# Kernel optimization log

Measured on AMD Instinct MI355X. Metric: run time of the kernel, lower is better.

Reference implementation:

```python
import jax, jax.numpy as jnp
import numpy as np

B, S, D, H = 2, 2048, 1024, 16
DK = D // H

def setup_inputs() -> dict:
    key = jax.random.key(0)
    ks = jax.random.split(key, 12)
    s = 1.0 / np.sqrt(D)
    return {
        "q": jax.random.normal(ks[0], (B, S, D), jnp.float32),
        "k": jax.random.normal(ks[1], (B, S, D), jnp.float32),
        "v": jax.random.normal(ks[2], (B, S, D), jnp.float32),
        "mask": jnp.ones((1, 1, S, S), jnp.int32),
        "Wq": jax.random.normal(ks[3], (D, D), jnp.float32) * s,
        "bq": jnp.zeros((D,), jnp.float32),
        "Wk": jax.random.normal(ks[4], (D, D), jnp.float32) * s,
        "bk": jnp.zeros((D,), jnp.float32),
        "Wv": jax.random.normal(ks[5], (D, D), jnp.float32) * s,
        "bv": jnp.zeros((D,), jnp.float32),
        "Wo": jax.random.normal(ks[6], (D, D), jnp.float32) * s,
        "bo": jnp.zeros((D,), jnp.float32),
    }

def reference(q, k, v, mask, Wq, bq, Wk, bk, Wv, bv, Wo, bo):
    # projections (torch Linear: x @ W^T + b)
    Q = q @ Wq.T + bq
    K = k @ Wk.T + bk
    V = v @ Wv.T + bv
    # split heads: [B,S,D] -> [B,H,S,DK]
    def split(x):
        return x.reshape(B, S, H, DK).transpose(0, 2, 1, 3)
    Qh, Kh, Vh = split(Q), split(K), split(V)
    scores = jnp.einsum('bhqd,bhkd->bhqk', Qh, Kh) / jnp.sqrt(jnp.float32(DK))
    scores = jnp.where(mask == 0, jnp.float32(-1e9), scores)
    attn = jax.nn.softmax(scores, axis=-1)  # dropout p=0.0 -> identity
    x = jnp.einsum('bhqk,bhkd->bhqd', attn, Vh)
    x = x.transpose(0, 2, 1, 3).reshape(B, S, D)
    return x @ Wo.T + bo
```

## Files before the change

kernel.cpp:

```cpp
#include <hip/hip_runtime.h>
#include <hip/hip_bf16.h>
#include <stdint.h>

#define B_    2
#define S_    2048
#define D_    1024
#define H_    16
#define NTOK  (B_ * S_)

typedef __attribute__((ext_vector_type(8))) short bf16x8;
typedef __attribute__((ext_vector_type(4))) float f32x4;
typedef __attribute__((ext_vector_type(2))) float float2v;
typedef __attribute__((ext_vector_type(2))) __bf16 bfv2;

static __device__ __forceinline__ unsigned int pkbf(float a, float b) {
    float2v fv = {a, b};
    bfv2 r = __builtin_convertvector(fv, bfv2);
    unsigned int u;
    __builtin_memcpy(&u, &r, 4);
    return u;
}

using g_cu32 = __attribute__((address_space(1))) const unsigned int;
using l_u32  = __attribute__((address_space(3))) unsigned int;
static __device__ __forceinline__ void gld16(const void* g, void* l) {
    __builtin_amdgcn_global_load_lds((g_cu32*)g, (l_u32*)l, 16, 0, 0);
}

template<int N> static __device__ __forceinline__ void wait_vm() {
    if constexpr (N == 0)      asm volatile("s_waitcnt vmcnt(0)" ::: "memory");
    else if constexpr (N == 2) asm volatile("s_waitcnt vmcnt(2)" ::: "memory");
    else if constexpr (N == 3) asm volatile("s_waitcnt vmcnt(3)" ::: "memory");
    else if constexpr (N == 4) asm volatile("s_waitcnt vmcnt(4)" ::: "memory");
    else if constexpr (N == 6) asm volatile("s_waitcnt vmcnt(6)" ::: "memory");
}
static __device__ __forceinline__ void wait_lgkm0() {
    asm volatile("s_waitcnt lgkmcnt(0)" ::: "memory");
}

#define QN ((size_t)NTOK * D_)
#define WN ((size_t)D_ * D_)

struct SwapT { static constexpr bool value = true; };
struct NoSwapT { static constexpr bool value = false; };

__global__ __launch_bounds__(256) void prep_kernel(
    const float* __restrict__ q, const float* __restrict__ k, const float* __restrict__ v,
    const float* __restrict__ Wq, const float* __restrict__ Wk,
    const float* __restrict__ Wv, const float* __restrict__ Wo,
    const int* __restrict__ mask,
    unsigned short* __restrict__ qb, unsigned short* __restrict__ kb,
    unsigned short* __restrict__ vb, unsigned short* __restrict__ wqb,
    unsigned short* __restrict__ wkb, unsigned short* __restrict__ wvb,
    unsigned short* __restrict__ wob, int* __restrict__ flags) {
    __shared__ int anyz;
    if (blockIdx.x < 8192) {
        size_t i = ((size_t)blockIdx.x * 256 + threadIdx.x) * 8;
        const float* s; unsigned short* d; size_t off;
        if (i < QN)          { s = q; d = qb; off = i; }
        else if (i < 2 * QN) { s = k; d = kb; off = i - QN; }
        else if (i < 3 * QN) { s = v; d = vb; off = i - 2 * QN; }
        else {
            size_t j = i - 3 * QN;
            int wi = (int)(j >> 20);
            s = (wi == 0) ? Wq : (wi == 1) ? Wk : (wi == 2) ? Wv : Wo;
            d = (wi == 0) ? wqb : (wi == 1) ? wkb : (wi == 2) ? wvb : wob;
            off = j & (WN - 1);
        }
        float4 a = *(const float4*)(s + off);
        float4 b = *(const float4*)(s + off + 4);
        uint4 pk;
        pk.x = pkbf(a.x, a.y); pk.y = pkbf(a.z, a.w);
        pk.z = pkbf(b.x, b.y); pk.w = pkbf(b.z, b.w);
        *(uint4*)(d + off) = pk;
    } else {
        if (threadIdx.x == 0) anyz = 0;
        __syncthreads();
        int bid2 = blockIdx.x - 8192;
        const int qt = bid2 >> 5, kt = bid2 & 31;
        int az = 0;
        for (int i = threadIdx.x; i < 64 * 64; i += 256) {
            int r = i >> 6, c = i & 63;
            az |= (mask[(size_t)(qt * 64 + r) * S_ + kt * 64 + c] == 0) ? 1 : 0;
        }
        if (az) atomicOr(&anyz, 1);
        __syncthreads();
        if (threadIdx.x == 0) flags[qt * 32 + kt] = anyz;
    }
}

struct GemmArgs {
    const unsigned short* A[3];
    const unsigned short* W[3];
    const float* bias[3];
    void* C[3];
    int mode[3];
    float scale[3];
};

__global__ __launch_bounds__(128, 3) void gemm_n64(GemmArgs ga) {
    constexpr int NK = D_ / 32;
    constexpr int AG = 8;
    constexpr int NG = 12;
    constexpr int GPW = 6;
    const int bid = blockIdx.x;
    const int l = (bid & 7) * 192 + (bid >> 3);
    const int z = l >> 9;
    const int r = l & 511;
    const int bx = r & 31;
    const int by = r >> 5;

    const unsigned short* __restrict__ A = ga.A[z];
    const unsigned short* __restrict__ W = ga.W[z];
    const float* __restrict__ bias = ga.bias[z];
    void* C = ga.C[z];
    const int mode = ga.mode[z];
    const float scl = ga.scale[z];

    __shared__ unsigned short Ls[2][NG * 512];

    const int t    = threadIdx.x;
    const int lane = t & 63;
    const int w    = t >> 6;
    const int fr   = lane & 15;
    const int kq   = lane >> 4;
    const int m0 = bx * 128, n0 = by * 64;

    const int sc = lane >> 4;
    const int sr = lane & 15;

    const unsigned short* gp[GPW];
    int ldo[GPW];
#pragma unroll
    for (int j = 0; j < GPW; ++j) {
        int g = w * GPW + j;
        if (g < AG) gp[j] = A + (size_t)(m0 + g * 16 + sr) * D_ + sc * 8;
        else        gp[j] = W + (size_t)(n0 + (g - AG) * 16 + sr) * D_ + sc * 8;
        ldo[j] = g * 512;
    }

    int aOff[4], bOff[4];
#pragma unroll
    for (int mi = 0; mi < 4; ++mi) aOff[mi] = (w * 4 + mi) * 512 + (kq * 16 + fr) * 8;
#pragma unroll
    for (int ni = 0; ni < 4; ++ni) bOff[ni] = (AG + ni) * 512 + (kq * 16 + fr) * 8;

    f32x4 acc[4][4];
#pragma unroll
    for (int i = 0; i < 4; ++i)
#pragma unroll
        for (int j = 0; j < 4; ++j) acc[i][j] = (f32x4)0.0f;

    auto stage = [&](int buf) {
#pragma unroll
        for (int j = 0; j < GPW; ++j) {
            gld16(gp[j], &Ls[buf][ldo[j]]);
            gp[j] += 32;
        }
    };

    auto kloop = [&](auto swc) {
        constexpr bool SW = decltype(swc)::value;
        stage(0);
        stage(1);
        for (int k0 = 0; k0 < NK; ++k0) {
            const int cur = k0 & 1;
            __builtin_amdgcn_sched_barrier(0);
            if (k0 < NK - 1) wait_vm<GPW>();
            else             wait_vm<0>();
            __builtin_amdgcn_s_barrier();
            __builtin_amdgcn_sched_barrier(0);

            bf16x8 af[4], bfr[4];
#pragma unroll
            for (int mi = 0; mi < 4; ++mi) af[mi] = *(const bf16x8*)&Ls[cur][aOff[mi]];
#pragma unroll
            for (int ni = 0; ni < 4; ++ni) bfr[ni] = *(const bf16x8*)&Ls[cur][bOff[ni]];

            wait_lgkm0();
            __builtin_amdgcn_sched_barrier(0);
            __builtin_amdgcn_s_barrier();
            if (k0 + 2 < NK) stage(cur);

#pragma unroll
            for (int mi = 0; mi < 4; ++mi)
#pragma unroll
                for (int ni = 0; ni < 4; ++ni) {
                    if constexpr (SW)
                        acc[mi][ni] = __builtin_amdgcn_mfma_f32_16x16x32_bf16(
                            bfr[ni], af[mi], acc[mi][ni], 0, 0, 0);
                    else
                        acc[mi][ni] = __builtin_amdgcn_mfma_f32_16x16x32_bf16(
                            af[mi], bfr[ni], acc[mi][ni], 0, 0, 0);
                }
        }
    };
    if (mode == 2) kloop(NoSwapT{}); else kloop(SwapT{});

    if (mode == 2) {
        unsigned short* Co = (unsigned short*)C;
#pragma unroll
        for (int ni = 0; ni < 4; ++ni) {
            int col = n0 + ni * 16 + fr;
            float bv = bias[col];
            int hh = col >> 6, d = col & 63;
#pragma unroll
            for (int mi = 0; mi < 4; ++mi) {
                int tok = m0 + w * 64 + mi * 16 + kq * 4;
                int bb = tok >> 11, sbase = tok & (S_ - 1);
                uint2 pk;
                pk.x = pkbf((acc[mi][ni][0] + bv) * scl, (acc[mi][ni][1] + bv) * scl);
                pk.y = pkbf((acc[mi][ni][2] + bv) * scl, (acc[mi][ni][3] + bv) * scl);
                *(uint2*)(Co + ((size_t)((bb * H_ + hh) * 64 + d)) * S_ + sbase) = pk;
            }
        }
    } else {
        unsigned short* Co = (unsigned short*)C;
#pragma unroll
        for (int ni = 0; ni < 4; ++ni) {
            int nb = n0 + ni * 16 + kq * 4;
            float4 b4 = *(const float4*)&bias[nb];
#pragma unroll
            for (int mi = 0; mi < 4; ++mi) {
                int m = m0 + w * 64 + mi * 16 + fr;
                uint2 pk;
                pk.x = pkbf((acc[mi][ni][0] + b4.x) * scl, (acc[mi][ni][1] + b4.y) * scl);
                pk.y = pkbf((acc[mi][ni][2] + b4.z) * scl, (acc[mi][ni][3] + b4.w) * scl);
                *(uint2*)(Co + (size_t)m * D_ + nb) = pk;
            }
        }
    }
}

template<int BMT>
__global__ __launch_bounds__(256, 3) void gemm_async(GemmArgs ga) {
    constexpr int AG = BMT / 16;
    constexpr int MI = BMT / 32;
    constexpr int NK = D_ / 32;
    constexpr int LOADS = (BMT == 128) ? 4 : 3;
    constexpr int MT = NTOK / BMT;
    constexpr int PERZ = MT * 8;

    const int bid = blockIdx.x;
    const int nb8 = (int)gridDim.x >> 3;
    const int l = (bid & 7) * nb8 + (bid >> 3);
    const int z = l / PERZ;
    const int r = l % PERZ;
    const int bx = r % MT;
    const int by = r / MT;

    const unsigned short* __restrict__ A = ga.A[z];
    const unsigned short* __restrict__ W = ga.W[z];
    const float* __restrict__ bias = ga.bias[z];
    void* C = ga.C[z];
    const float scl = ga.scale[z];

    __shared__ unsigned short As[3][AG * 512];
    __shared__ unsigned short Bs[3][8 * 512];

    const int t    = threadIdx.x;
    const int lane = t & 63;
    const int w    = t >> 6;
    const int fr   = lane & 15;
    const int kq   = lane >> 4;
    const int wrow = w >> 1, wcol = w & 1;
    const int m0 = bx * BMT, n0 = by * 128;

    const int sc = lane >> 4;
    const int sr = lane & 15;

    const unsigned short* ga0 = A + (size_t)(m0 + w * 16 + sr) * D_ + sc * 8;
    const int la0Off = w * 512;
    const unsigned short* gw0 = W + (size_t)(n0 + (2 * w) * 16 + sr) * D_ + sc * 8;
    const unsigned short* gw1 = gw0 + 16 * D_;
    const int lw0Off = (2 * w) * 512;
    const int lw1Off = (2 * w + 1) * 512;

    int aOff[MI], bOff[4];
#pragma unroll
    for (int mi = 0; mi < MI; ++mi) aOff[mi] = (wrow * MI + mi) * 512 + (kq * 16 + fr) * 8;
#pragma unroll
    for (int ni = 0; ni < 4; ++ni) bOff[ni] = (wcol * 4 + ni) * 512 + (kq * 16 + fr) * 8;

    f32x4 acc[MI][4];
#pragma unroll
    for (int i = 0; i < MI; ++i)
#pragma unroll
        for (int j = 0; j < 4; ++j) acc[i][j] = (f32x4)0.0f;

    auto stage = [&](int buf) {
        gld16(ga0, &As[buf][la0Off]);
        gld16(gw0, &Bs[buf][lw0Off]);
        gld16(gw1, &Bs[buf][lw1Off]);
        ga0 += 32; gw0 += 32; gw1 += 32;
    };

    auto mma_step = [&](int cur) {
        const unsigned short* Ab = As[cur];
        const unsigned short* Bb = Bs[cur];
        bf16x8 af[MI], bfr[4];
#pragma unroll
        for (int mi = 0; mi < MI; ++mi) af[mi] = *(const bf16x8*)&Ab[aOff[mi]];
#pragma unroll
        for (int ni = 0; ni < 4; ++ni) bfr[ni] = *(const bf16x8*)&Bb[bOff[ni]];
#pragma unroll
        for (int mi = 0; mi < MI; ++mi)
#pragma unroll
            for (int ni = 0; ni < 4; ++ni)
                acc[mi][ni] = __builtin_amdgcn_mfma_f32_16x16x32_bf16(
                    bfr[ni], af[mi], acc[mi][ni], 0, 0, 0);
    };

    stage(0);
    stage(1);
    int cur = 0;
    for (int k0 = 0; k0 < NK - 1; ++k0) {
        __builtin_amdgcn_sched_barrier(0);
        wait_vm<LOADS>();
        __builtin_amdgcn_s_barrier();
        __builtin_amdgcn_sched_barrier(0);
        if (k0 + 2 < NK) {
            int pf = (cur >= 1) ? cur - 1 : cur + 2;
            stage(pf);
        }
        mma_step(cur);
        cur = (cur < 2) ? cur + 1 : 0;
    }
    __builtin_amdgcn_sched_barrier(0);
    wait_vm<0>();
    __builtin_amdgcn_s_barrier();
    __builtin_amdgcn_sched_barrier(0);
    mma_step(cur);

    float* Co = (float*)C;
#pragma unroll
    for (int ni = 0; ni < 4; ++ni) {
        int nb = n0 + wcol * 64 + ni * 16 + kq * 4;
        float4 b4 = *(const float4*)&bias[nb];
#pragma unroll
        for (int mi = 0; mi < MI; ++mi) {
            int m = m0 + wrow * (BMT / 2) + mi * 16 + fr;
            float4 o4;
            o4.x = (acc[mi][ni][0] + b4.x) * scl;
            o4.y = (acc[mi][ni][1] + b4.y) * scl;
            o4.z = (acc[mi][ni][2] + b4.z) * scl;
            o4.w = (acc[mi][ni][3] + b4.w) * scl;
            *(float4*)(Co + (size_t)m * D_ + nb) = o4;
        }
    }
}

__global__ __launch_bounds__(512, 2) void flash4(
    const unsigned short* __restrict__ Qb, const unsigned short* __restrict__ Kb,
    const unsigned short* __restrict__ Vtg, const int* __restrict__ mask,
    const int* __restrict__ flags, unsigned short* __restrict__ Xb) {
    __shared__ unsigned short Ks[3][4096];
    __shared__ unsigned short Vs[3][4096];
    __shared__ unsigned short Ps[16384];

    const int t    = threadIdx.x;
    const int lane = t & 63;
    const int w    = t >> 6;
    const int fr   = lane & 15;
    const int kq   = lane >> 4;
    const int bid = blockIdx.x;
    const int swb = ((bid & 7) << 5) | (bid >> 3);
    const int qt = swb & 7, hd = (swb >> 3) & 15, b = swb >> 7;
    const int q0 = qt * 256;
    const int swz = fr & 7;

    bf16x8 qf[2][2];
#pragma unroll
    for (int qc = 0; qc < 2; ++qc) {
        const unsigned short* qrow_p =
            Qb + (size_t)(b * S_ + q0 + w * 32 + qc * 16 + fr) * D_ + hd * 64;
        qf[qc][0] = *(const bf16x8*)(qrow_p + kq * 8);
        qf[qc][1] = *(const bf16x8*)(qrow_p + 32 + kq * 8);
    }

    unsigned int fmask[2];
#pragma unroll
    for (int qc = 0; qc < 2; ++qc) {
        int qt64 = qt * 4 + ((2 * w + qc) >> 2);
        int fl = (lane < 32) ? flags[qt64 * 32 + lane] : 0;
        fmask[qc] = (unsigned int)__ballot(fl != 0);
    }

    const unsigned short* kptr =
        Kb + (size_t)(b * S_ + (w >> 1) * 16 + fr) * D_ + hd * 64 + (w & 1) * 32 + kq * 8;
    const unsigned short* vptr =
        Vtg + ((size_t)((b * H_ + hd) * 64 + (w >> 1) * 16 + fr)) * S_ + (w & 1) * 32 + kq * 8;

    gld16(kptr, (char*)&Ks[0][0] + w * 1024);
    gld16(vptr, (char*)&Vs[0][0] + w * 1024);
    gld16(kptr + (size_t)64 * D_, (char*)&Ks[1][0] + w * 1024);
    gld16(vptr + 64,              (char*)&Vs[1][0] + w * 1024);
    const unsigned short* kpf = kptr + (size_t)128 * D_;
    const unsigned short* vpf = vptr + 128;

    unsigned short* pswr[2][4];
    const unsigned short* psrd[2][2];
#pragma unroll
    for (int qc = 0; qc < 2; ++qc) {
        int row = w * 32 + qc * 16 + fr;
#pragma unroll
        for (int mi = 0; mi < 4; ++mi) {
            int chunk = mi * 2 + (kq >> 1);
            pswr[qc][mi] = &Ps[row * 64 + ((chunk ^ swz) << 3) + ((kq & 1) << 2)];
        }
#pragma unroll
        for (int kk = 0; kk < 2; ++kk) {
            int c = kk * 4 + kq;
            psrd[qc][kk] = &Ps[row * 64 + ((c ^ swz) << 3)];
        }
    }

    const f32x4 zf = (f32x4)0.0f;
    f32x4 o[2][4];
#pragma unroll
    for (int qc = 0; qc < 2; ++qc)
#pragma unroll
        for (int i = 0; i < 4; ++i) o[qc][i] = zf;
    float2v l2[2];
    l2[0] = (float2v){0.0f, 0.0f};
    l2[1] = (float2v){0.0f, 0.0f};

    auto attn_step = [&](int cur, int kt) {
        f32x4 st[2][4];
#pragma unroll
        for (int mi = 0; mi < 4; ++mi) {
            bf16x8 a = *(const bf16x8*)&Ks[cur][mi * 1024 + (kq * 16 + fr) * 8];
            st[0][mi] = __builtin_amdgcn_mfma_f32_16x16x32_bf16(a, qf[0][0], zf, 0, 0, 0);
            st[1][mi] = __builtin_amdgcn_mfma_f32_16x16x32_bf16(a, qf[1][0], zf, 0, 0, 0);
        }
#pragma unroll
        for (int mi = 0; mi < 4; ++mi) {
            bf16x8 a = *(const bf16x8*)&Ks[cur][mi * 1024 + ((4 + kq) * 16 + fr) * 8];
            st[0][mi] = __builtin_amdgcn_mfma_f32_16x16x32_bf16(a, qf[0][1], st[0][mi], 0, 0, 0);
            st[1][mi] = __builtin_amdgcn_mfma_f32_16x16x32_bf16(a, qf[1][1], st[1][mi], 0, 0, 0);
        }

#pragma unroll
        for (int qc = 0; qc < 2; ++qc) {
            if ((fmask[qc] >> kt) & 1u) {
#pragma unroll
                for (int mi = 0; mi < 4; ++mi) {
                    int4 mv = *(const int4*)&mask[(size_t)(q0 + w * 32 + qc * 16 + fr) * S_ +
                                                  kt * 64 + mi * 16 + kq * 4];
                    if (mv.x == 0) st[qc][mi][0] = -3e8f;
                    if (mv.y == 0) st[qc][mi][1] = -3e8f;
                    if (mv.z == 0) st[qc][mi][2] = -3e8f;
                    if (mv.w == 0) st[qc][mi][3] = -3e8f;
                }
            }
        }

#pragma unroll
        for (int qc = 0; qc < 2; ++qc)
#pragma unroll
            for (int mi = 0; mi < 4; ++mi) {
                float e0 = __builtin_amdgcn_exp2f(st[qc][mi][0]);
                float e1 = __builtin_amdgcn_exp2f(st[qc][mi][1]);
                float e2 = __builtin_amdgcn_exp2f(st[qc][mi][2]);
                float e3 = __builtin_amdgcn_exp2f(st[qc][mi][3]);
                l2[qc] += (float2v){e0, e1} + (float2v){e2, e3};
                uint2 pk;
                pk.x = pkbf(e0, e1);
                pk.y = pkbf(e2, e3);
                *(uint2*)pswr[qc][mi] = pk;
            }

#pragma unroll
        for (int kk = 0; kk < 2; ++kk) {
            bf16x8 pb0 = *(const bf16x8*)psrd[0][kk];
            bf16x8 pb1 = *(const bf16x8*)psrd[1][kk];
#pragma unroll
            for (int mi = 0; mi < 4; ++mi) {
                bf16x8 a = *(const bf16x8*)&Vs[cur][mi * 1024 + ((kk * 4 + kq) * 16 + fr) * 8];
                o[0][mi] = __builtin_amdgcn_mfma_f32_16x16x32_bf16(a, pb0, o[0][mi], 0, 0, 0);
                o[1][mi] = __builtin_amdgcn_mfma_f32_16x16x32_bf16(a, pb1, o[1][mi], 0, 0, 0);
            }
        }
    };

    int cur = 0;
    for (int kt = 0; kt < 31; ++kt) {
        __builtin_amdgcn_sched_barrier(0);
        wait_vm<2>();
        __builtin_amdgcn_s_barrier();
        __builtin_amdgcn_sched_barrier(0);
        if (kt < 30) {
            int pf = (cur >= 1) ? cur - 1 : cur + 2;
            gld16(kpf, (char*)&Ks[pf][0] + w * 1024);
            gld16(vpf, (char*)&Vs[pf][0] + w * 1024);
            kpf += (size_t)64 * D_;
            vpf += 64;
        }
        attn_step(cur, kt);
        cur = (cur < 2) ? cur + 1 : 0;
    }
    __builtin_amdgcn_sched_barrier(0);
    wait_vm<0>();
    __builtin_amdgcn_s_barrier();
    __builtin_amdgcn_sched_barrier(0);
    attn_step(cur, 31);

#pragma unroll
    for (int qc = 0; qc < 2; ++qc) {
        float l_i = l2[qc].x + l2[qc].y;
        l_i += __shfl_xor(l_i, 16, 64);
        l_i += __shfl_xor(l_i, 32, 64);
        float rl = 1.0f / l_i;
#pragma unroll
        for (int mi = 0; mi < 4; ++mi) {
            uint2 pk;
            pk.x = pkbf(o[qc][mi][0] * rl, o[qc][mi][1] * rl);
            pk.y = pkbf(o[qc][mi][2] * rl, o[qc][mi][3] * rl);
            *(uint2*)(Xb + (size_t)(b * S_ + q0 + w * 32 + qc * 16 + fr) * D_ +
                      hd * 64 + mi * 16 + kq * 4) = pk;
        }
    }
}

extern "C" void kernel_launch(void* const* d_in, const int* in_sizes, int n_in,
                              void* d_out, int out_size, void* d_ws, size_t ws_size,
                              hipStream_t stream) {
    const float* q    = (const float*)d_in[0];
    const float* k    = (const float*)d_in[1];
    const float* v    = (const float*)d_in[2];
    const int*   mask = (const int*)d_in[3];
    const float* Wq   = (const float*)d_in[4];
    const float* bq   = (const float*)d_in[5];
    const float* Wk   = (const float*)d_in[6];
    const float* bk   = (const float*)d_in[7];
    const float* Wv   = (const float*)d_in[8];
    const float* bv   = (const float*)d_in[9];
    const float* Wo   = (const float*)d_in[10];
    const float* bo   = (const float*)d_in[11];
    float* out = (float*)d_out;

    unsigned short* qb  = (unsigned short*)d_ws;
    unsigned short* kb  = qb + QN;
    unsigned short* vb  = kb + QN;
    unsigned short* Qf  = vb + QN;
    unsigned short* Kf  = Qf + QN;
    unsigned short* Vt  = Kf + QN;
    unsigned short* wqb = Vt + QN;
    unsigned short* wkb = wqb + WN;
    unsigned short* wvb = wkb + WN;
    unsigned short* wob = wvb + WN;
    int* flags = (int*)(wob + WN);

    const float SC = 0.18033688011112042f;

    prep_kernel<<<9216, 256, 0, stream>>>(q, k, v, Wq, Wk, Wv, Wo, mask,
                                          qb, kb, vb, wqb, wkb, wvb, wob, flags);

    GemmArgs g1;
    g1.A[0] = qb;  g1.W[0] = wqb; g1.bias[0] = bq; g1.C[0] = Qf; g1.mode[0] = 1; g1.scale[0] = SC;
    g1.A[1] = kb;  g1.W[1] = wkb; g1.bias[1] = bk; g1.C[1] = Kf; g1.mode[1] = 1; g1.scale[1] = 1.0f;
    g1.A[2] = vb;  g1.W[2] = wvb; g1.bias[2] = bv; g1.C[2] = Vt; g1.mode[2] = 2; g1.scale[2] = 1.0f;
    gemm_n64<<<1536, 128, 0, stream>>>(g1);

    flash4<<<256, 512, 0, stream>>>(Qf, Kf, Vt, mask, flags, Qf);

    GemmArgs g2;
    g2.A[0] = Qf; g2.W[0] = wob; g2.bias[0] = bo; g2.C[0] = out; g2.mode[0] = 0; g2.scale[0] = 1.0f;
    g2.A[1] = g2.A[2] = nullptr; g2.W[1] = g2.W[2] = nullptr;
    g2.bias[1] = g2.bias[2] = nullptr; g2.C[1] = g2.C[2] = nullptr;
    g2.mode[1] = g2.mode[2] = 0; g2.scale[1] = g2.scale[2] = 1.0f;
    gemm_async<64><<<512, 256, 0, stream>>>(g2);
}
```

Baseline: 285.4 us.

## Enlarge QKV and output projection GEMM tiles with triple-buffered async loads

The QKV projection GEMM moves from 128x64 tiles with 2-wave blocks to 256x128 tiles with 8-wave blocks and a triple-buffered LDS pipeline. This removes the second barrier per k-step and increases data reuse per block. The output projection moves from 64-row to 128-row tiles, with 256 blocks instead of 512. Larger tiles cut global and LDS traffic per FLOP, but leave fewer blocks, so CU occupancy may fall: 384 and 256 blocks on a GPU with roughly 256 CUs.

```diff
diff --git a/kernel.cpp b/kernel.cpp
--- a/kernel.cpp
+++ b/kernel.cpp
@@ -32,17 +32,10 @@
     else if constexpr (N == 2) asm volatile("s_waitcnt vmcnt(2)" ::: "memory");
     else if constexpr (N == 3) asm volatile("s_waitcnt vmcnt(3)" ::: "memory");
     else if constexpr (N == 4) asm volatile("s_waitcnt vmcnt(4)" ::: "memory");
-    else if constexpr (N == 6) asm volatile("s_waitcnt vmcnt(6)" ::: "memory");
-}
-static __device__ __forceinline__ void wait_lgkm0() {
-    asm volatile("s_waitcnt lgkmcnt(0)" ::: "memory");
 }
 
 #define QN ((size_t)NTOK * D_)
 #define WN ((size_t)D_ * D_)
-
-struct SwapT { static constexpr bool value = true; };
-struct NoSwapT { static constexpr bool value = false; };
 
 __global__ __launch_bounds__(256) void prep_kernel(
     const float* __restrict__ q, const float* __restrict__ k, const float* __restrict__ v,
@@ -98,17 +91,17 @@
     float scale[3];
 };
 
-__global__ __launch_bounds__(128, 3) void gemm_n64(GemmArgs ga) {
+__global__ __launch_bounds__(512, 2) void gemm_bigM(GemmArgs ga) {
     constexpr int NK = D_ / 32;
-    constexpr int AG = 8;
-    constexpr int NG = 12;
-    constexpr int GPW = 6;
+    constexpr int AG = 16;
+    constexpr int NG = 24;
+
     const int bid = blockIdx.x;
-    const int l = (bid & 7) * 192 + (bid >> 3);
-    const int z = l >> 9;
-    const int r = l & 511;
-    const int bx = r & 31;
-    const int by = r >> 5;
+    const int l = (bid & 7) * 48 + (bid >> 3);
+    const int z = l >> 7;
+    const int r = l & 127;
+    const int bx = r & 15;
+    const int by = r >> 4;
 
     const unsigned short* __restrict__ A = ga.A[z];
     const unsigned short* __restrict__ W = ga.W[z];
@@ -117,33 +110,30 @@
     const int mode = ga.mode[z];
     const float scl = ga.scale[z];
 
-    __shared__ unsigned short Ls[2][NG * 512];
+    __shared__ unsigned short Ls[3][NG * 512];
 
     const int t    = threadIdx.x;
     const int lane = t & 63;
     const int w    = t >> 6;
     const int fr   = lane & 15;
     const int kq   = lane >> 4;
-    const int m0 = bx * 128, n0 = by * 64;
+    const int wrow = w >> 1;
+    const int wcol = w & 1;
+    const int m0 = bx * 256, n0 = by * 128;
 
     const int sc = lane >> 4;
     const int sr = lane & 15;
 
-    const unsigned short* gp[GPW];
-    int ldo[GPW];
-#pragma unroll
-    for (int j = 0; j < GPW; ++j) {
-        int g = w * GPW + j;
-        if (g < AG) gp[j] = A + (size_t)(m0 + g * 16 + sr) * D_ + sc * 8;
-        else        gp[j] = W + (size_t)(n0 + (g - AG) * 16 + sr) * D_ + sc * 8;
-        ldo[j] = g * 512;
-    }
+    const unsigned short* gA0 = A + (size_t)(m0 + (2 * w) * 16 + sr) * D_ + sc * 8;
+    const unsigned short* gA1 = gA0 + 16 * D_;
+    const unsigned short* gB0 = W + (size_t)(n0 + w * 16 + sr) * D_ + sc * 8;
+    const int lA0 = (2 * w) * 512, lA1 = (2 * w + 1) * 512, lB0 = (AG + w) * 512;
 
     int aOff[4], bOff[4];
 #pragma unroll
-    for (int mi = 0; mi < 4; ++mi) aOff[mi] = (w * 4 + mi) * 512 + (kq * 16 + fr) * 8;
-#pragma unroll
-    for (int ni = 0; ni < 4; ++ni) bOff[ni] = (AG + ni) * 512 + (kq * 16 + fr) * 8;
+    for (int mi = 0; mi < 4; ++mi) aOff[mi] = (wrow * 4 + mi) * 512 + (kq * 16 + fr) * 8;
+#pragma unroll
+    for (int ni = 0; ni < 4; ++ni) bOff[ni] = (AG + wcol * 4 + ni) * 512 + (kq * 16 + fr) * 8;
 
     f32x4 acc[4][4];
 #pragma unroll
@@ -152,61 +142,61 @@
         for (int j = 0; j < 4; ++j) acc[i][j] = (f32x4)0.0f;
 
     auto stage = [&](int buf) {
-#pragma unroll
-        for (int j = 0; j < GPW; ++j) {
-            gld16(gp[j], &Ls[buf][ldo[j]]);
-            gp[j] += 32;
-        }
+        gld16(gA0, &Ls[buf][lA0]);
+        gld16(gA1, &Ls[buf][lA1]);
+        gld16(gB0, &Ls[buf][lB0]);
+        gA0 += 32; gA1 += 32; gB0 += 32;
     };
 
-    auto kloop = [&](auto swc) {
-        constexpr bool SW = decltype(swc)::value;
-        stage(0);
-        stage(1);
-        for (int k0 = 0; k0 < NK; ++k0) {
-            const int cur = k0 & 1;
-            __builtin_amdgcn_sched_barrier(0);
-            if (k0 < NK - 1) wait_vm<GPW>();
-            else             wait_vm<0>();
-            __builtin_amdgcn_s_barrier();
-            __builtin_amdgcn_sched_barrier(0);
-
-            bf16x8 af[4], bfr[4];
-#pragma unroll
-            for (int mi = 0; mi < 4; ++mi) af[mi] = *(const bf16x8*)&Ls[cur][aOff[mi]];
-#pragma unroll
-            for (int ni = 0; ni < 4; ++ni) bfr[ni] = *(const bf16x8*)&Ls[cur][bOff[ni]];
-
-            wait_lgkm0();
-            __builtin_amdgcn_sched_barrier(0);
-            __builtin_amdgcn_s_barrier();
-            if (k0 + 2 < NK) stage(cur);
-
+    const bool swp = (mode != 2);
+
+    stage(0);
+    stage(1);
+    int cur = 0;
+    for (int k0 = 0; k0 < NK; ++k0) {
+        __builtin_amdgcn_sched_barrier(0);
+        if (k0 < NK - 1) wait_vm<3>();
+        else             wait_vm<0>();
+        __builtin_amdgcn_s_barrier();
+        __builtin_amdgcn_sched_barrier(0);
+        if (k0 + 2 < NK) {
+            int pf = (cur >= 1) ? cur - 1 : cur + 2;
+            stage(pf);
+        }
+
+        bf16x8 af[4], bfr[4];
+#pragma unroll
+        for (int mi = 0; mi < 4; ++mi) af[mi] = *(const bf16x8*)&Ls[cur][aOff[mi]];
+#pragma unroll
+        for (int ni = 0; ni < 4; ++ni) bfr[ni] = *(const bf16x8*)&Ls[cur][bOff[ni]];
+        if (swp) {
 #pragma unroll
             for (int mi = 0; mi < 4; ++mi)
 #pragma unroll
-                for (int ni = 0; ni < 4; ++ni) {
-                    if constexpr (SW)
-                        acc[mi][ni] = __builtin_amdgcn_mfma_f32_16x16x32_bf16(
-                            bfr[ni], af[mi], acc[mi][ni], 0, 0, 0);
-                    else
-                        acc[mi][ni] = __builtin_amdgcn_mfma_f32_16x16x32_bf16(
-                            af[mi], bfr[ni], acc[mi][ni], 0, 0, 0);
-                }
-        }
-    };
-    if (mode == 2) kloop(NoSwapT{}); else kloop(SwapT{});
+                for (int ni = 0; ni < 4; ++ni)
+                    acc[mi][ni] = __builtin_amdgcn_mfma_f32_16x16x32_bf16(
+                        bfr[ni], af[mi], acc[mi][ni], 0, 0, 0);
+        } else {
+#pragma unroll
+            for (int mi = 0; mi < 4; ++mi)
+#pragma unroll
+                for (int ni = 0; ni < 4; ++ni)
+                    acc[mi][ni] = __builtin_amdgcn_mfma_f32_16x16x32_bf16(
+                        af[mi], bfr[ni], acc[mi][ni], 0, 0, 0);
+        }
+        cur = (cur < 2) ? cur + 1 : 0;
+    }
 
     if (mode == 2) {
         unsigned short* Co = (unsigned short*)C;
 #pragma unroll
         for (int ni = 0; ni < 4; ++ni) {
-            int col = n0 + ni * 16 + fr;
+            int col = n0 + wcol * 64 + ni * 16 + fr;
             float bv = bias[col];
             int hh = col >> 6, d = col & 63;
 #pragma unroll
             for (int mi = 0; mi < 4; ++mi) {
-                int tok = m0 + w * 64 + mi * 16 + kq * 4;
+                int tok = m0 + wrow * 64 + mi * 16 + kq * 4;
                 int bb = tok >> 11, sbase = tok & (S_ - 1);
                 uint2 pk;
                 pk.x = pkbf((acc[mi][ni][0] + bv) * scl, (acc[mi][ni][1] + bv) * scl);
@@ -218,11 +208,11 @@
         unsigned short* Co = (unsigned short*)C;
 #pragma unroll
         for (int ni = 0; ni < 4; ++ni) {
-            int nb = n0 + ni * 16 + kq * 4;
+            int nb = n0 + wcol * 64 + ni * 16 + kq * 4;
             float4 b4 = *(const float4*)&bias[nb];
 #pragma unroll
             for (int mi = 0; mi < 4; ++mi) {
-                int m = m0 + w * 64 + mi * 16 + fr;
+                int m = m0 + wrow * 64 + mi * 16 + fr;
                 uint2 pk;
                 pk.x = pkbf((acc[mi][ni][0] + b4.x) * scl, (acc[mi][ni][1] + b4.y) * scl);
                 pk.y = pkbf((acc[mi][ni][2] + b4.z) * scl, (acc[mi][ni][3] + b4.w) * scl);
@@ -232,30 +222,19 @@
     }
 }
 
-template<int BMT>
-__global__ __launch_bounds__(256, 3) void gemm_async(GemmArgs ga) {
-    constexpr int AG = BMT / 16;
-    constexpr int MI = BMT / 32;
+__global__ __launch_bounds__(256, 3) void gemm_out(GemmArgs ga) {
     constexpr int NK = D_ / 32;
-    constexpr int LOADS = (BMT == 128) ? 4 : 3;
-    constexpr int MT = NTOK / BMT;
-    constexpr int PERZ = MT * 8;
-
     const int bid = blockIdx.x;
-    const int nb8 = (int)gridDim.x >> 3;
-    const int l = (bid & 7) * nb8 + (bid >> 3);
-    const int z = l / PERZ;
-    const int r = l % PERZ;
-    const int bx = r % MT;
-    const int by = r / MT;
-
-    const unsigned short* __restrict__ A = ga.A[z];
-    const unsigned short* __restrict__ W = ga.W[z];
-    const float* __restrict__ bias = ga.bias[z];
-    void* C = ga.C[z];
-    const float scl = ga.scale[z];
-
-    __shared__ unsigned short As[3][AG * 512];
+    const int l = (bid & 7) * 32 + (bid >> 3);
+    const int bx = l & 31;
+    const int by = l >> 5;
+
+    const unsigned short* __restrict__ A = ga.A[0];
+    const unsigned short* __restrict__ W = ga.W[0];
+    const float* __restrict__ bias = ga.bias[0];
+    float* Co = (float*)ga.C[0];
+
+    __shared__ unsigned short As[3][8 * 512];
     __shared__ unsigned short Bs[3][8 * 512];
 
     const int t    = threadIdx.x;
@@ -264,87 +243,78 @@
     const int fr   = lane & 15;
     const int kq   = lane >> 4;
     const int wrow = w >> 1, wcol = w & 1;
-    const int m0 = bx * BMT, n0 = by * 128;
+    const int m0 = bx * 128, n0 = by * 128;
 
     const int sc = lane >> 4;
     const int sr = lane & 15;
 
-    const unsigned short* ga0 = A + (size_t)(m0 + w * 16 + sr) * D_ + sc * 8;
-    const int la0Off = w * 512;
+    const unsigned short* ga0 = A + (size_t)(m0 + (2 * w) * 16 + sr) * D_ + sc * 8;
+    const unsigned short* ga1 = ga0 + 16 * D_;
     const unsigned short* gw0 = W + (size_t)(n0 + (2 * w) * 16 + sr) * D_ + sc * 8;
     const unsigned short* gw1 = gw0 + 16 * D_;
-    const int lw0Off = (2 * w) * 512;
-    const int lw1Off = (2 * w + 1) * 512;
-
-    int aOff[MI], bOff[4];
-#pragma unroll
-    for (int mi = 0; mi < MI; ++mi) aOff[mi] = (wrow * MI + mi) * 512 + (kq * 16 + fr) * 8;
+    const int la0 = (2 * w) * 512, la1 = (2 * w + 1) * 512;
+    const int lw0 = (2 * w) * 512, lw1 = (2 * w + 1) * 512;
+
+    int aOff[4], bOff[4];
+#pragma unroll
+    for (int mi = 0; mi < 4; ++mi) aOff[mi] = (wrow * 4 + mi) * 512 + (kq * 16 + fr) * 8;
 #pragma unroll
     for (int ni = 0; ni < 4; ++ni) bOff[ni] = (wcol * 4 + ni) * 512 + (kq * 16 + fr) * 8;
 
-    f32x4 acc[MI][4];
-#pragma unroll
-    for (int i = 0; i < MI; ++i)
+    f32x4 acc[4][4];
+#pragma unroll
+    for (int i = 0; i < 4; ++i)
 #pragma unroll
         for (int j = 0; j < 4; ++j) acc[i][j] = (f32x4)0.0f;
 
     auto stage = [&](int buf) {
-        gld16(ga0, &As[buf][la0Off]);
-        gld16(gw0, &Bs[buf][lw0Off]);
-        gld16(gw1, &Bs[buf][lw1Off]);
-        ga0 += 32; gw0 += 32; gw1 += 32;
-    };
-
-    auto mma_step = [&](int cur) {
-        const unsigned short* Ab = As[cur];
-        const unsigned short* Bb = Bs[cur];
-        bf16x8 af[MI], bfr[4];
-#pragma unroll
-        for (int mi = 0; mi < MI; ++mi) af[mi] = *(const bf16x8*)&Ab[aOff[mi]];
-#pragma unroll
-        for (int ni = 0; ni < 4; ++ni) bfr[ni] = *(const bf16x8*)&Bb[bOff[ni]];
-#pragma unroll
-        for (int mi = 0; mi < MI; ++mi)
-#pragma unroll
-            for (int ni = 0; ni < 4; ++ni)
-                acc[mi][ni] = __builtin_amdgcn_mfma_f32_16x16x32_bf16(
-                    bfr[ni], af[mi], acc[mi][ni], 0, 0, 0);
+        gld16(ga0, &As[buf][la0]);
+        gld16(ga1, &As[buf][la1]);
+        gld16(gw0, &Bs[buf][lw0]);
+        gld16(gw1, &Bs[buf][lw1]);
+        ga0 += 32; ga1 += 32; gw0 += 32; gw1 += 32;
     };
 
     stage(0);
     stage(1);
     int cur = 0;
-    for (int k0 = 0; k0 < NK - 1; ++k0) {
+    for (int k0 = 0; k0 < NK; ++k0) {
         __builtin_amdgcn_sched_barrier(0);
-        wait_vm<LOADS>();
+        if (k0 < NK - 1) wait_vm<4>();
+        else             wait_vm<0>();
         __builtin_amdgcn_s_barrier();
         __builtin_amdgcn_sched_barrier(0);
         if (k0 + 2 < NK) {
             int pf = (cur >= 1) ? cur - 1 : cur + 2;
             stage(pf);
         }
-        mma_step(cur);
+
+        bf16x8 af[4], bfr[4];
+#pragma unroll
+        for (int mi = 0; mi < 4; ++mi) af[mi] = *(const bf16x8*)&As[cur][aOff[mi]];
+#pragma unroll
+        for (int ni = 0; ni < 4; ++ni) bfr[ni] = *(const bf16x8*)&Bs[cur][bOff[ni]];
+#pragma unroll
+        for (int mi = 0; mi < 4; ++mi)
+#pragma unroll
+            for (int ni = 0; ni < 4; ++ni)
+                acc[mi][ni] = __builtin_amdgcn_mfma_f32_16x16x32_bf16(
+                    bfr[ni], af[mi], acc[mi][ni], 0, 0, 0);
         cur = (cur < 2) ? cur + 1 : 0;
     }
-    __builtin_amdgcn_sched_barrier(0);
-    wait_vm<0>();
-    __builtin_amdgcn_s_barrier();
-    __builtin_amdgcn_sched_barrier(0);
-    mma_step(cur);
-
-    float* Co = (float*)C;
+
 #pragma unroll
     for (int ni = 0; ni < 4; ++ni) {
         int nb = n0 + wcol * 64 + ni * 16 + kq * 4;
         float4 b4 = *(const float4*)&bias[nb];
 #pragma unroll
-        for (int mi = 0; mi < MI; ++mi) {
-            int m = m0 + wrow * (BMT / 2) + mi * 16 + fr;
+        for (int mi = 0; mi < 4; ++mi) {
+            int m = m0 + wrow * 64 + mi * 16 + fr;
             float4 o4;
-            o4.x = (acc[mi][ni][0] + b4.x) * scl;
-            o4.y = (acc[mi][ni][1] + b4.y) * scl;
-            o4.z = (acc[mi][ni][2] + b4.z) * scl;
-            o4.w = (acc[mi][ni][3] + b4.w) * scl;
+            o4.x = acc[mi][ni][0] + b4.x;
+            o4.y = acc[mi][ni][1] + b4.y;
+            o4.z = acc[mi][ni][2] + b4.z;
+            o4.w = acc[mi][ni][3] + b4.w;
             *(float4*)(Co + (size_t)m * D_ + nb) = o4;
         }
     }
@@ -560,7 +530,7 @@
     g1.A[0] = qb;  g1.W[0] = wqb; g1.bias[0] = bq; g1.C[0] = Qf; g1.mode[0] = 1; g1.scale[0] = SC;
     g1.A[1] = kb;  g1.W[1] = wkb; g1.bias[1] = bk; g1.C[1] = Kf; g1.mode[1] = 1; g1.scale[1] = 1.0f;
     g1.A[2] = vb;  g1.W[2] = wvb; g1.bias[2] = bv; g1.C[2] = Vt; g1.mode[2] = 2; g1.scale[2] = 1.0f;
-    gemm_n64<<<1536, 128, 0, stream>>>(g1);
+    gemm_bigM<<<384, 512, 0, stream>>>(g1);
 
     flash4<<<256, 512, 0, stream>>>(Qf, Kf, Vt, mask, flags, Qf);
 
@@ -569,5 +539,5 @@
     g2.A[1] = g2.A[2] = nullptr; g2.W[1] = g2.W[2] = nullptr;
     g2.bias[1] = g2.bias[2] = nullptr; g2.C[1] = g2.C[2] = nullptr;
     g2.mode[1] = g2.mode[2] = 0; g2.scale[1] = g2.scale[2] = 1.0f;
-    gemm_async<64><<<512, 256, 0, stream>>>(g2);
-}
+    gemm_out<<<256, 256, 0, stream>>>(g2);
+}
```

After: 272.8 us. 4.4% less time.
